# Kernel optimization log

Hardware: AMD Instinct MI355X
Metric: run time of the kernel (lower is better)

The kernel has to match this reference:

```python
import jax, jax.numpy as jnp
import numpy as np

LATENT = 1024
HIDDEN = 4096
ENC = 1024
HEADS = 16
HEAD_DIM = LATENT // HEADS
B, SQ, SK = 4, 1024, 1024
EPS = 1e-5


def _linear(x, w, b):
    # torch nn.Linear: y = x @ w.T + b, w shape (out, in)
    return jnp.einsum('bsi,oi->bso', x, w) + b


def _mha(Q, K, wq, bq, wk, bk, wv, bv, wo, bo):
    Bq, Sq, _ = Q.shape
    Sk = K.shape[1]
    Qp = _linear(Q, wq, bq).reshape(Bq, Sq, HEADS, HEAD_DIM)
    Kp = _linear(K, wk, bk).reshape(Bq, Sk, HEADS, HEAD_DIM)
    Vp = _linear(K, wv, bv).reshape(Bq, Sk, HEADS, HEAD_DIM)
    # NOTE: original scales by 1/sqrt(latent_size), not 1/sqrt(head_dim)
    E = jnp.einsum('bqhd,bkhd->bhqk', Qp, Kp) / np.sqrt(LATENT).astype(np.float32)
    A = jax.nn.softmax(E, axis=-1)
    O = jnp.einsum('bhqk,bkhd->bqhd', A, Vp).reshape(Bq, Sq, LATENT)
    return _linear(O, wo, bo)


def _ln(x, g, b):
    mu = jnp.mean(x, axis=-1, keepdims=True)
    var = jnp.mean((x - mu) ** 2, axis=-1, keepdims=True)
    return (x - mu) * jax.lax.rsqrt(var + EPS) * g + b


def setup_inputs() -> dict:
    key = jax.random.key(0)
    ks = jax.random.split(key, 32)
    s = 0.02
    d = {
        'Q': jax.random.normal(ks[0], (B, SQ, LATENT), jnp.float32),
        'K': jax.random.normal(ks[1], (B, SK, ENC), jnp.float32),
        'a1_wq': jax.random.normal(ks[2], (LATENT, LATENT)) * s,
        'a1_bq': jnp.zeros((LATENT,)),
        'a1_wk': jax.random.normal(ks[3], (LATENT, LATENT)) * s,
        'a1_bk': jnp.zeros((LATENT,)),
        'a1_wv': jax.random.normal(ks[4], (LATENT, LATENT)) * s,
        'a1_bv': jnp.zeros((LATENT,)),
        'a1_wo': jax.random.normal(ks[5], (LATENT, LATENT)) * s,
        'a1_bo': jnp.zeros((LATENT,)),
        'a2_wq': jax.random.normal(ks[6], (LATENT, LATENT)) * s,
        'a2_bq': jnp.zeros((LATENT,)),
        'a2_wk': jax.random.normal(ks[7], (LATENT, ENC)) * s,
        'a2_bk': jnp.zeros((LATENT,)),
        'a2_wv': jax.random.normal(ks[8], (LATENT, ENC)) * s,
        'a2_bv': jnp.zeros((LATENT,)),
        'a2_wo': jax.random.normal(ks[9], (LATENT, LATENT)) * s,
        'a2_bo': jnp.zeros((LATENT,)),
        'fc_w1': jax.random.normal(ks[10], (HIDDEN, LATENT)) * s,
        'fc_b1': jnp.zeros((HIDDEN,)),
        'fc_w2': jax.random.normal(ks[11], (LATENT, HIDDEN)) * s,
        'fc_b2': jnp.zeros((LATENT,)),
        'ln0_g': jnp.ones((LATENT,)), 'ln0_b': jnp.zeros((LATENT,)),
        'ln1_g': jnp.ones((LATENT,)), 'ln1_b': jnp.zeros((LATENT,)),
        'ln2_g': jnp.ones((LATENT,)), 'ln2_b': jnp.zeros((LATENT,)),
    }
    return d


def reference(Q, K, a1_wq, a1_bq, a1_wk, a1_bk, a1_wv, a1_bv, a1_wo, a1_bo,
              a2_wq, a2_bq, a2_wk, a2_bk, a2_wv, a2_bv, a2_wo, a2_bo,
              fc_w1, fc_b1, fc_w2, fc_b2,
              ln0_g, ln0_b, ln1_g, ln1_b, ln2_g, ln2_b):
    # self-attention block
    A1 = _mha(Q, Q, a1_wq, a1_bq, a1_wk, a1_bk, a1_wv, a1_bv, a1_wo, a1_bo)
    X = _ln(Q + A1, ln0_g, ln0_b)
    # cross-attention block
    A2 = _mha(X, K, a2_wq, a2_bq, a2_wk, a2_bk, a2_wv, a2_bv, a2_wo, a2_bo)
    X = _ln(X + A2, ln1_g, ln1_b)
    # FFN: Linear -> ReLU -> Linear
    FC = _linear(jax.nn.relu(_linear(X, fc_w1, fc_b1)), fc_w2, fc_b2)
    X = _ln(X + FC, ln2_g, ln2_b)
    return X
```

## Files before the change

### kernel.cpp

```cpp
#include <hip/hip_runtime.h>
#include <hip/hip_bf16.h>
#include <math.h>

#define LATENT 1024
#define HIDDEN 4096
#define HEADS 16
#define HEAD_DIM 64
#define BATCH 4
#define SQL 1024
#define SKL 1024

typedef __bf16 bf16;
typedef __attribute__((ext_vector_type(4))) __bf16 bf16x4;
typedef __attribute__((ext_vector_type(8))) __bf16 bf16x8;
typedef __attribute__((ext_vector_type(4))) float f32x4;

#define MFMA16 __builtin_amdgcn_mfma_f32_16x16x32_bf16

__device__ __forceinline__ void async_ld16(const bf16* g, bf16* l) {
    __builtin_amdgcn_global_load_lds(
        (const __attribute__((address_space(1))) unsigned int*)g,
        (__attribute__((address_space(3))) unsigned int*)l,
        16, 0, 0);
}

__global__ void detect_dtype(const void* g, int* flag) {
    if (threadIdx.x == 0) *flag = (*(const float*)g == 1.0f) ? 1 : 0;
}

struct CanonArgs {
    const void* src[28];
    bf16* dst[28];
    int n[28];
};

__global__ __launch_bounds__(256) void canonicalize(CanonArgs a, const int* flagp) {
    const int buf = blockIdx.y;
    const int n = a.n[buf];
    const int i0 = (blockIdx.x * 256 + threadIdx.x) * 8;
    if (i0 >= n) return;
    bf16* dst = a.dst[buf];
    if (*flagp) {
        const float* s = (const float*)a.src[buf];
        float4 u0 = *(const float4*)(s + i0);
        float4 u1 = *(const float4*)(s + i0 + 4);
        bf16x8 o;
        o[0] = (bf16)u0.x; o[1] = (bf16)u0.y; o[2] = (bf16)u0.z; o[3] = (bf16)u0.w;
        o[4] = (bf16)u1.x; o[5] = (bf16)u1.y; o[6] = (bf16)u1.z; o[7] = (bf16)u1.w;
        *(bf16x8*)(dst + i0) = o;
    } else {
        *(bf16x8*)(dst + i0) = *(const bf16x8*)((const bf16*)a.src[buf] + i0);
    }
}

template<int BN, bool RELU>
__global__ __launch_bounds__(256, 2)
void gemm2(const bf16* __restrict__ A, const bf16* __restrict__ W,
           const bf16* __restrict__ bias,
           bf16* __restrict__ out0, bf16* __restrict__ out1, bf16* __restrict__ outT,
           int M, int N, int K, int nNormal, int ostride) {
    constexpr int WAVES_N = BN / 64;
    constexpr int WAVES_M = 4 / WAVES_N;
    constexpr int WM = 128 / WAVES_M;
    constexpr int MI = WM / 16;
    constexpr int BROWS = BN / 4;
    constexpr int BUFSZ = (128 + BN) * 64;
    __shared__ alignas(16) bf16 smem[2 * BUFSZ];
    const int tid  = threadIdx.x;
    const int w    = tid >> 6;
    const int lane = tid & 63;
    const int quad = lane >> 4;
    const int l16  = lane & 15;
    const int bm = blockIdx.y * 128;
    const int bn = blockIdx.x * BN;
    const int wr = w / WAVES_N, wc = w % WAVES_N;

    f32x4 acc[MI][4] = {};

    const int srow = lane >> 3;
    const int schk = (lane & 7) * 8;
    const bf16* Abase = A + (long)(bm + w * 32 + srow) * K + schk;
    const bf16* Wbase = W + (long)(bn + w * BROWS + srow) * K + schk;
    const int lAoff = (w * 32 + srow) * 64 + schk;
    const int lBoff = 128 * 64 + (w * BROWS + srow) * 64 + schk;

#define STAGE_G(bufp, kk)                                                      \
    {                                                                          \
        bf16* bb_ = smem + (bufp) * BUFSZ;                                     \
        _Pragma("unroll")                                                      \
        for (int i_ = 0; i_ < 4; ++i_)                                         \
            async_ld16(Abase + (kk) + (long)(i_ * 8) * K, bb_ + lAoff + i_ * 8 * 64); \
        _Pragma("unroll")                                                      \
        for (int i_ = 0; i_ < BROWS / 8; ++i_)                                 \
            async_ld16(Wbase + (kk) + (long)(i_ * 8) * K, bb_ + lBoff + i_ * 8 * 64); \
    }

    STAGE_G(0, 0);
    __asm__ volatile("s_waitcnt vmcnt(0)" ::: "memory");
    __builtin_amdgcn_s_barrier();
    __builtin_amdgcn_sched_barrier(0);

    int cur = 0;
    for (int k0 = 0; k0 < K; k0 += 64) {
        if (k0 + 64 < K) STAGE_G(cur ^ 1, k0 + 64);
        const bf16* lA = smem + cur * BUFSZ;
        const bf16* lB = lA + 128 * 64;
#pragma unroll
        for (int ks = 0; ks < 2; ++ks) {
            bf16x8 af[MI], bfv[4];
#pragma unroll
            for (int i = 0; i < MI; ++i)
                af[i] = *(const bf16x8*)&lA[(wr * WM + i * 16 + l16) * 64 + ks * 32 + quad * 8];
#pragma unroll
            for (int j = 0; j < 4; ++j)
                bfv[j] = *(const bf16x8*)&lB[(wc * 64 + j * 16 + l16) * 64 + ks * 32 + quad * 8];
#pragma unroll
            for (int i = 0; i < MI; ++i)
#pragma unroll
                for (int j = 0; j < 4; ++j)
                    acc[i][j] = MFMA16(af[i], bfv[j], acc[i][j], 0, 0, 0);
        }
        __asm__ volatile("s_waitcnt vmcnt(0)" ::: "memory");
        __builtin_amdgcn_s_barrier();
        __builtin_amdgcn_sched_barrier(0);
        cur ^= 1;
    }
#undef STAGE_G

    float bvv[4];
#pragma unroll
    for (int j = 0; j < 4; ++j) bvv[j] = (float)bias[bn + wc * 64 + j * 16 + l16];

    if (bn < nNormal) {
        bf16* base = out0;
        int colb = bn;
        if (out1 && colb >= 1024) { base = out1; colb -= 1024; }
#pragma unroll
        for (int i = 0; i < MI; ++i) {
#pragma unroll
            for (int r = 0; r < 4; ++r) {
                const int row = bm + wr * WM + i * 16 + quad * 4 + r;
#pragma unroll
                for (int j = 0; j < 4; ++j) {
                    float v = acc[i][j][r] + bvv[j];
                    if (RELU) v = fmaxf(v, 0.f);
                    base[(long)row * ostride + colb + wc * 64 + j * 16 + l16] = (bf16)v;
                }
            }
        }
    } else {
        const int n0v = bn - nNormal;
        __syncthreads();
#pragma unroll
        for (int p = 0; p < 2; ++p) {
            if (p) __syncthreads();
            if (wc == p) {
#pragma unroll
                for (int i = 0; i < MI; ++i)
#pragma unroll
                    for (int j = 0; j < 4; ++j) {
                        const int colL = j * 16 + l16;
                        const int rowL = wr * WM + i * 16 + quad * 4;
                        bf16x4 pk;
#pragma unroll
                        for (int r = 0; r < 4; ++r) pk[r] = (bf16)(acc[i][j][r] + bvv[j]);
                        *(bf16x4*)&smem[colL * 136 + rowL] = pk;
                    }
            }
            __syncthreads();
#pragma unroll
            for (int k = 0; k < 8; ++k) {
                const int c = tid + k * 256;
                const int rL = c >> 5, ch = c & 31;
                *(bf16x4*)&outT[(long)(n0v + p * 64 + rL) * M + bm + ch * 4] =
                    *(const bf16x4*)&smem[rL * 136 + ch * 4];
            }
        }
    }
}

__global__ __launch_bounds__(256, 3)
void attn2(const bf16* __restrict__ Qp, const bf16* __restrict__ Kp,
           const bf16* __restrict__ Vt, bf16* __restrict__ O) {
    __shared__ alignas(16) bf16 lQ[64 * 64];
    __shared__ alignas(16) bf16 lK[2][64 * 64];
    __shared__ alignas(16) bf16 lV[2][64 * 64];
    __shared__ alignas(16) bf16 lP[4][16 * 64];
    const int tid  = threadIdx.x;
    const int w    = tid >> 6;
    const int lane = tid & 63;
    const int quad = lane >> 4;
    const int l16  = lane & 15;
    const int b  = blockIdx.z;
    const int h  = blockIdx.y;
    const int q0 = blockIdx.x * 64;

#pragma unroll
    for (int s = 0; s < 2; ++s) {
        const int c = w * 128 + s * 64 + lane;
        const int row = c >> 3, ch = (c & 7) * 8;
        async_ld16(Qp + (long)(b * SQL + q0 + row) * LATENT + h * 64 + ch, lQ + c * 8);
    }
#define STAGE_KV(buf, kt)                                                        \
    {                                                                            \
        _Pragma("unroll")                                                        \
        for (int s = 0; s < 2; ++s) {                                            \
            const int c = w * 128 + s * 64 + lane;                               \
            const int row = c >> 3, ch = (c & 7) * 8;                            \
            async_ld16(Kp + (long)(b * SKL + (kt) * 64 + row) * LATENT + h * 64 + ch, \
                       &lK[buf][c * 8]);                                         \
            async_ld16(Vt + (long)(h * 64 + row) * (BATCH * SKL) + b * SKL + (kt) * 64 + ch, \
                       &lV[buf][c * 8]);                                         \
        }                                                                        \
    }
    STAGE_KV(0, 0);
    __syncthreads();

    bf16x8 aq[2];
    aq[0] = *(const bf16x8*)&lQ[(w * 16 + l16) * 64 + quad * 8];
    aq[1] = *(const bf16x8*)&lQ[(w * 16 + l16) * 64 + 32 + quad * 8];

    f32x4 o_acc[4] = {};
    float lsum[4] = {0.f, 0.f, 0.f, 0.f};

    for (int kt = 0; kt < SKL / 64; ++kt) {
        const int cur = kt & 1;
        if (kt < SKL / 64 - 1) STAGE_KV(cur ^ 1, kt + 1);

        f32x4 s4[4] = {};
#pragma unroll
        for (int ks = 0; ks < 2; ++ks)
#pragma unroll
            for (int j = 0; j < 4; ++j) {
                bf16x8 bk = *(const bf16x8*)&lK[cur][(j * 16 + l16) * 64 + ks * 32 + quad * 8];
                s4[j] = MFMA16(aq[ks], bk, s4[j], 0, 0, 0);
            }

#pragma unroll
        for (int r = 0; r < 4; ++r)
#pragma unroll
            for (int j = 0; j < 4; ++j) {
                const float p = __expf(s4[j][r] * 0.03125f);
                lsum[r] += p;
                lP[w][(quad * 4 + r) * 64 + j * 16 + l16] = (bf16)p;
            }
        __asm__ volatile("s_waitcnt lgkmcnt(0)" ::: "memory");

#pragma unroll
        for (int ks = 0; ks < 2; ++ks) {
            bf16x8 ap = *(const bf16x8*)&lP[w][l16 * 64 + ks * 32 + quad * 8];
#pragma unroll
            for (int j = 0; j < 4; ++j) {
                bf16x8 bv = *(const bf16x8*)&lV[cur][(j * 16 + l16) * 64 + ks * 32 + quad * 8];
                o_acc[j] = MFMA16(ap, bv, o_acc[j], 0, 0, 0);
            }
        }
        __syncthreads();
    }

#pragma unroll
    for (int r = 0; r < 4; ++r) {
#pragma unroll
        for (int off = 1; off <= 8; off <<= 1)
            lsum[r] += __shfl_xor(lsum[r], off, 64);
    }
#pragma unroll
    for (int r = 0; r < 4; ++r) {
        const float inv = 1.f / lsum[r];
        const int row = q0 + w * 16 + quad * 4 + r;
#pragma unroll
        for (int j = 0; j < 4; ++j)
            O[(long)(b * SQL + row) * LATENT + h * 64 + j * 16 + l16] = (bf16)(o_acc[j][r] * inv);
    }
#undef STAGE_KV
}

template<bool F32OUT>
__global__ __launch_bounds__(256)
void ln_kernel(const bf16* __restrict__ res, const bf16* __restrict__ y,
               const bf16* __restrict__ g, const bf16* __restrict__ bta,
               bf16* __restrict__ outres, void* __restrict__ outb) {
    const int row = blockIdx.x;
    const int tid = threadIdx.x;
    const long base = (long)row * LATENT;
    const int c = tid * 4;
    bf16x4 rv = *(const bf16x4*)&res[base + c];
    bf16x4 yv = *(const bf16x4*)&y[base + c];
    float x[4];
    float s1 = 0.f, s2 = 0.f;
#pragma unroll
    for (int i = 0; i < 4; ++i) {
        float v = (float)rv[i] + (float)yv[i];
        x[i] = v; s1 += v; s2 += v * v;
    }
#pragma unroll
    for (int off = 32; off >= 1; off >>= 1) {
        s1 += __shfl_xor(s1, off, 64);
        s2 += __shfl_xor(s2, off, 64);
    }
    __shared__ float ps1[4], ps2[4];
    const int w = tid >> 6, lane = tid & 63;
    if (lane == 0) { ps1[w] = s1; ps2[w] = s2; }
    __syncthreads();
    s1 = ps1[0] + ps1[1] + ps1[2] + ps1[3];
    s2 = ps2[0] + ps2[1] + ps2[2] + ps2[3];
    const float mu = s1 * (1.f / LATENT);
    const float var = s2 * (1.f / LATENT) - mu * mu;
    const float rstd = rsqrtf(var + 1e-5f);
    bf16x4 gv = *(const bf16x4*)&g[c];
    bf16x4 bv = *(const bf16x4*)&bta[c];
    float o[4];
#pragma unroll
    for (int i = 0; i < 4; ++i)
        o[i] = (x[i] - mu) * rstd * (float)gv[i] + (float)bv[i];
    if (F32OUT) {
        float4 f; f.x = o[0]; f.y = o[1]; f.z = o[2]; f.w = o[3];
        *(float4*)&((float*)outb)[base + c] = f;
    } else {
        bf16x4 bo;
#pragma unroll
        for (int i = 0; i < 4; ++i) bo[i] = (bf16)o[i];
        *(bf16x4*)&((bf16*)outb)[base + c] = bo;
        if (outres) *(bf16x4*)&outres[base + c] = bo;
    }
}

extern "C" void kernel_launch(void* const* d_in, const int* in_sizes, int n_in,
                              void* d_out, int out_size, void* d_ws, size_t ws_size,
                              hipStream_t stream) {
    char* ws = (char*)d_ws;

    static const int order[28] = {2, 4, 6, 3, 5, 7, 12, 14, 13, 15,
                                  0, 1, 8, 9, 10, 11, 16, 17, 18, 19,
                                  20, 21, 22, 23, 24, 25, 26, 27};
    size_t coff[28];
    size_t cur = 256;
    for (int k = 0; k < 28; ++k) {
        const int i = order[k];
        coff[i] = cur;
        cur += (((size_t)in_sizes[i] * 2) + 255) & ~(size_t)255;
    }
    const size_t canon_end = (cur + 255) & ~(size_t)255;
    const size_t MB8 = 8ull << 20;
    const size_t need = canon_end + 7 * MB8;
    const bool full = ws_size >= need;

    const bf16* cv[28];
    if (full) {
        int* flag = (int*)ws;
        detect_dtype<<<dim3(1), dim3(64), 0, stream>>>(d_in[22], flag);
        CanonArgs ca;
        for (int i = 0; i < 28; ++i) {
            ca.src[i] = d_in[i];
            ca.dst[i] = (bf16*)(ws + coff[i]);
            ca.n[i]   = in_sizes[i];
            cv[i]     = (const bf16*)(ws + coff[i]);
        }
        canonicalize<<<dim3(2048, 28), dim3(256), 0, stream>>>(ca, flag);
    } else {
        for (int i = 0; i < 28; ++i) cv[i] = (const bf16*)d_in[i];
    }

    const size_t base = full ? canon_end : 0;
    bf16* Xres = (bf16*)(ws + base);
    bf16* Yf   = (bf16*)(ws + base + 1 * MB8);
    bf16* Xb   = (bf16*)(ws + base + 2 * MB8);
    bf16* Qp   = (bf16*)(ws + base + 3 * MB8);
    bf16* Kp   = (bf16*)(ws + base + 4 * MB8);
    bf16* Vt   = (bf16*)(ws + base + 5 * MB8);
    bf16* AttO = (bf16*)(ws + base + 6 * MB8);
    bf16* H    = Qp;

    const bf16 *Qc = cv[0], *Kc = cv[1];
    const int M = BATCH * SQL;
    dim3 blk(256);
    dim3 ga(SQL / 64, HEADS, BATCH);

    gemm2<128, false><<<dim3(3072 / 128, M / 128), blk, 0, stream>>>(
        Qc, cv[2], cv[3], Qp, Kp, Vt, M, 3072, LATENT, 2048, 1024);
    attn2<<<ga, blk, 0, stream>>>(Qp, Kp, Vt, AttO);
    gemm2<64, false><<<dim3(1024 / 64, M / 128), blk, 0, stream>>>(
        AttO, cv[8], cv[9], Yf, nullptr, nullptr, M, 1024, LATENT, 1024, 1024);
    ln_kernel<false><<<dim3(M), blk, 0, stream>>>(Qc, Yf, cv[22], cv[23], Xres, Xb);

    gemm2<64, false><<<dim3(1024 / 64, M / 128), blk, 0, stream>>>(
        Xb, cv[10], cv[11], Qp, nullptr, nullptr, M, 1024, LATENT, 1024, 1024);
    gemm2<128, false><<<dim3(2048 / 128, M / 128), blk, 0, stream>>>(
        Kc, cv[12], cv[13], Kp, nullptr, Vt, M, 2048, LATENT, 1024, 1024);
    attn2<<<ga, blk, 0, stream>>>(Qp, Kp, Vt, AttO);
    gemm2<64, false><<<dim3(1024 / 64, M / 128), blk, 0, stream>>>(
        AttO, cv[16], cv[17], Yf, nullptr, nullptr, M, 1024, LATENT, 1024, 1024);
    ln_kernel<false><<<dim3(M), blk, 0, stream>>>(Xres, Yf, cv[24], cv[25], Xres, Xb);

    gemm2<128, true><<<dim3(4096 / 128, M / 128), blk, 0, stream>>>(
        Xb, cv[18], cv[19], H, nullptr, nullptr, M, HIDDEN, LATENT, 4096, 4096);
    gemm2<64, false><<<dim3(1024 / 64, M / 128), blk, 0, stream>>>(
        H, cv[20], cv[21], Yf, nullptr, nullptr, M, 1024, HIDDEN, 1024, 1024);
    ln_kernel<true><<<dim3(M), blk, 0, stream>>>(Xres, Yf, cv[26], cv[27], nullptr, d_out);
}
```

Measured before the change: 520.5 us.

## Triple-buffer GEMM K-loop with 32-wide swizzled LDS tiles and higher occupancy

Restructures the bf16 GEMM main loop to use BK=32 tiles in a three-stage ring of LDS buffers. Each thread issues async global-to-LDS loads two stages ahead and waits with partial vmcnt counts, so loads overlap compute instead of draining every iteration. LDS rows are XOR-swizzled to avoid bank conflicts on the MFMA fragment reads. Launch bounds are raised to 3-4 blocks per CU. The trade-off is twice as many barriers per K, plus register pressure under the tighter occupancy bound.

```diff
diff --git a/kernel.cpp b/kernel.cpp
--- a/kernel.cpp
+++ b/kernel.cpp
@@ -54,8 +54,8 @@
 }
 
 template<int BN, bool RELU>
-__global__ __launch_bounds__(256, 2)
-void gemm2(const bf16* __restrict__ A, const bf16* __restrict__ W,
+__global__ __launch_bounds__(256, (BN == 128) ? 3 : 4)
+void gemm4(const bf16* __restrict__ A, const bf16* __restrict__ W,
            const bf16* __restrict__ bias,
            bf16* __restrict__ out0, bf16* __restrict__ out1, bf16* __restrict__ outT,
            int M, int N, int K, int nNormal, int ostride) {
@@ -63,9 +63,12 @@
     constexpr int WAVES_M = 4 / WAVES_N;
     constexpr int WM = 128 / WAVES_M;
     constexpr int MI = WM / 16;
-    constexpr int BROWS = BN / 4;
-    constexpr int BUFSZ = (128 + BN) * 64;
-    __shared__ alignas(16) bf16 smem[2 * BUFSZ];
+    constexpr int ASLOT = 128 * 4;
+    constexpr int BSLOT = BN * 4;
+    constexpr int SLOTS = ASLOT + BSLOT;
+    constexpr int LPT   = SLOTS / 256;
+    constexpr int BUFE  = SLOTS * 8;
+    __shared__ alignas(16) bf16 smem[3 * BUFE];
     const int tid  = threadIdx.x;
     const int w    = tid >> 6;
     const int lane = tid & 63;
@@ -77,53 +80,71 @@
 
     f32x4 acc[MI][4] = {};
 
-    const int srow = lane >> 3;
-    const int schk = (lane & 7) * 8;
-    const bf16* Abase = A + (long)(bm + w * 32 + srow) * K + schk;
-    const bf16* Wbase = W + (long)(bn + w * BROWS + srow) * K + schk;
-    const int lAoff = (w * 32 + srow) * 64 + schk;
-    const int lBoff = 128 * 64 + (w * BROWS + srow) * 64 + schk;
-
-#define STAGE_G(bufp, kk)                                                      \
+    const bf16* gsrc[LPT]; int loff[LPT];
+#pragma unroll
+    for (int i = 0; i < LPT; ++i) {
+        const int s = tid + i * 256;
+        int row, cs;
+        const bf16* base;
+        if (s < ASLOT) { row = s >> 2;           cs = s & 3; base = A + (long)(bm + row) * K; }
+        else           { const int sb = s - ASLOT; row = sb >> 2; cs = sb & 3;
+                         base = W + (long)(bn + row) * K; }
+        const int cg = cs ^ ((row >> 1) & 3);
+        gsrc[i] = base + cg * 8;
+        loff[i] = s * 8;
+    }
+
+    int offA[MI], offB[4];
+#pragma unroll
+    for (int i = 0; i < MI; ++i) {
+        const int r = wr * WM + i * 16 + l16;
+        offA[i] = r * 32 + ((quad ^ ((r >> 1) & 3)) << 3);
+    }
+#pragma unroll
+    for (int j = 0; j < 4; ++j) {
+        const int r = wc * 64 + j * 16 + l16;
+        offB[j] = ASLOT * 8 + r * 32 + ((quad ^ ((r >> 1) & 3)) << 3);
+    }
+
+#define STAGE_G(dst, tt)                                                       \
     {                                                                          \
-        bf16* bb_ = smem + (bufp) * BUFSZ;                                     \
         _Pragma("unroll")                                                      \
-        for (int i_ = 0; i_ < 4; ++i_)                                         \
-            async_ld16(Abase + (kk) + (long)(i_ * 8) * K, bb_ + lAoff + i_ * 8 * 64); \
-        _Pragma("unroll")                                                      \
-        for (int i_ = 0; i_ < BROWS / 8; ++i_)                                 \
-            async_ld16(Wbase + (kk) + (long)(i_ * 8) * K, bb_ + lBoff + i_ * 8 * 64); \
-    }
-
-    STAGE_G(0, 0);
-    __asm__ volatile("s_waitcnt vmcnt(0)" ::: "memory");
+        for (int i_ = 0; i_ < LPT; ++i_)                                       \
+            async_ld16(gsrc[i_] + (tt) * 32, (dst) + loff[i_]);                \
+    }
+
+    const int NK = K >> 5;
+    bf16 *p0 = smem, *p1 = smem + BUFE, *p2 = smem + 2 * BUFE;
+    STAGE_G(p0, 0);
+    STAGE_G(p1, 1);
+    if constexpr (BN == 128) __asm__ volatile("s_waitcnt vmcnt(4)" ::: "memory");
+    else                     __asm__ volatile("s_waitcnt vmcnt(3)" ::: "memory");
     __builtin_amdgcn_s_barrier();
     __builtin_amdgcn_sched_barrier(0);
 
-    int cur = 0;
-    for (int k0 = 0; k0 < K; k0 += 64) {
-        if (k0 + 64 < K) STAGE_G(cur ^ 1, k0 + 64);
-        const bf16* lA = smem + cur * BUFSZ;
-        const bf16* lB = lA + 128 * 64;
-#pragma unroll
-        for (int ks = 0; ks < 2; ++ks) {
-            bf16x8 af[MI], bfv[4];
-#pragma unroll
-            for (int i = 0; i < MI; ++i)
-                af[i] = *(const bf16x8*)&lA[(wr * WM + i * 16 + l16) * 64 + ks * 32 + quad * 8];
+    for (int t = 0; t < NK; ++t) {
+        if (t + 2 < NK) STAGE_G(p2, t + 2);
+        bf16x8 af[MI], bfv[4];
+#pragma unroll
+        for (int i = 0; i < MI; ++i) af[i]  = *(const bf16x8*)&p0[offA[i]];
+#pragma unroll
+        for (int j = 0; j < 4; ++j) bfv[j] = *(const bf16x8*)&p0[offB[j]];
+#pragma unroll
+        for (int i = 0; i < MI; ++i)
 #pragma unroll
             for (int j = 0; j < 4; ++j)
-                bfv[j] = *(const bf16x8*)&lB[(wc * 64 + j * 16 + l16) * 64 + ks * 32 + quad * 8];
-#pragma unroll
-            for (int i = 0; i < MI; ++i)
-#pragma unroll
-                for (int j = 0; j < 4; ++j)
-                    acc[i][j] = MFMA16(af[i], bfv[j], acc[i][j], 0, 0, 0);
-        }
-        __asm__ volatile("s_waitcnt vmcnt(0)" ::: "memory");
-        __builtin_amdgcn_s_barrier();
-        __builtin_amdgcn_sched_barrier(0);
-        cur ^= 1;
+                acc[i][j] = MFMA16(af[i], bfv[j], acc[i][j], 0, 0, 0);
+        if (t + 2 < NK) {
+            if constexpr (BN == 128) __asm__ volatile("s_waitcnt vmcnt(4)" ::: "memory");
+            else                     __asm__ volatile("s_waitcnt vmcnt(3)" ::: "memory");
+        } else if (t + 1 < NK) {
+            __asm__ volatile("s_waitcnt vmcnt(0)" ::: "memory");
+        }
+        if (t + 1 < NK) {
+            __builtin_amdgcn_s_barrier();
+            __builtin_amdgcn_sched_barrier(0);
+        }
+        bf16* tp = p0; p0 = p1; p1 = p2; p2 = tp;
     }
 #undef STAGE_G
 
@@ -376,25 +397,25 @@
     dim3 blk(256);
     dim3 ga(SQL / 64, HEADS, BATCH);
 
-    gemm2<128, false><<<dim3(3072 / 128, M / 128), blk, 0, stream>>>(
+    gemm4<128, false><<<dim3(3072 / 128, M / 128), blk, 0, stream>>>(
         Qc, cv[2], cv[3], Qp, Kp, Vt, M, 3072, LATENT, 2048, 1024);
     attn2<<<ga, blk, 0, stream>>>(Qp, Kp, Vt, AttO);
-    gemm2<64, false><<<dim3(1024 / 64, M / 128), blk, 0, stream>>>(
+    gemm4<64, false><<<dim3(1024 / 64, M / 128), blk, 0, stream>>>(
         AttO, cv[8], cv[9], Yf, nullptr, nullptr, M, 1024, LATENT, 1024, 1024);
     ln_kernel<false><<<dim3(M), blk, 0, stream>>>(Qc, Yf, cv[22], cv[23], Xres, Xb);
 
-    gemm2<64, false><<<dim3(1024 / 64, M / 128), blk, 0, stream>>>(
+    gemm4<64, false><<<dim3(1024 / 64, M / 128), blk, 0, stream>>>(
         Xb, cv[10], cv[11], Qp, nullptr, nullptr, M, 1024, LATENT, 1024, 1024);
-    gemm2<128, false><<<dim3(2048 / 128, M / 128), blk, 0, stream>>>(
+    gemm4<128, false><<<dim3(2048 / 128, M / 128), blk, 0, stream>>>(
         Kc, cv[12], cv[13], Kp, nullptr, Vt, M, 2048, LATENT, 1024, 1024);
     attn2<<<ga, blk, 0, stream>>>(Qp, Kp, Vt, AttO);
-    gemm2<64, false><<<dim3(1024 / 64, M / 128), blk, 0, stream>>>(
+    gemm4<64, false><<<dim3(1024 / 64, M / 128), blk, 0, stream>>>(
         AttO, cv[16], cv[17], Yf, nullptr, nullptr, M, 1024, LATENT, 1024, 1024);
     ln_kernel<false><<<dim3(M), blk, 0, stream>>>(Xres, Yf, cv[24], cv[25], Xres, Xb);
 
-    gemm2<128, true><<<dim3(4096 / 128, M / 128), blk, 0, stream>>>(
+    gemm4<128, true><<<dim3(4096 / 128, M / 128), blk, 0, stream>>>(
         Xb, cv[18], cv[19], H, nullptr, nullptr, M, HIDDEN, LATENT, 4096, 4096);
-    gemm2<64, false><<<dim3(1024 / 64, M / 128), blk, 0, stream>>>(
+    gemm4<64, false><<<dim3(1024 / 64, M / 128), blk, 0, stream>>>(
         H, cv[20], cv[21], Yf, nullptr, nullptr, M, 1024, HIDDEN, 1024, 1024);
     ln_kernel<true><<<dim3(M), blk, 0, stream>>>(Xres, Yf, cv[26], cv[27], nullptr, d_out);
 }
```

Measured after the change: 520.4 us. About the same (-0.0%).

## Add 128x256 triple-buffered GEMM kernel for wide projection and FFN-up GEMMs

Applied to the files above, without the earlier changes.

Adds a new GEMM kernel with 128x256 output tiles, K-step 32, three LDS stages filled by async global-to-LDS loads, XOR-swizzled LDS layout, and an XCD-aware block remap. It replaces the 128x128 gemm2 for the fused QKV projection, the cross-attention KV projection and the FFN first layer. The larger tile raises arithmetic intensity per loaded byte, and deeper buffering aims to hide memory latency. In exchange it uses more accumulator registers (128 floats per thread) and gives fewer workgroups for the 2048-wide GEMM.

```diff
diff --git a/kernel.cpp b/kernel.cpp
--- a/kernel.cpp
+++ b/kernel.cpp
@@ -50,6 +50,153 @@
         *(bf16x8*)(dst + i0) = o;
     } else {
         *(bf16x8*)(dst + i0) = *(const bf16x8*)((const bf16*)a.src[buf] + i0);
+    }
+}
+
+template<bool RELU>
+__global__ __launch_bounds__(256, 2)
+void gemm8(const bf16* __restrict__ A, const bf16* __restrict__ W,
+           const bf16* __restrict__ bias,
+           bf16* __restrict__ out0, bf16* __restrict__ out1, bf16* __restrict__ outT,
+           int M, int N, int K, int nNormal, int ostride) {
+    constexpr int AE   = 128 * 32;
+    constexpr int BE   = 256 * 32;
+    constexpr int BUFE = AE + BE;
+    __shared__ alignas(16) bf16 smem[3 * BUFE];
+    const int tid  = threadIdx.x;
+    const int w    = tid >> 6;
+    const int lane = tid & 63;
+    const int quad = lane >> 4;
+    const int l16  = lane & 15;
+    const int wrr  = w >> 1, wcc = w & 1;
+    const int nx  = gridDim.x;
+    const int nwg = nx * gridDim.y;
+    int bid = blockIdx.y * nx + blockIdx.x;
+    bid = (bid & 7) * (nwg >> 3) + (bid >> 3);
+    const int bm = (bid / nx) * 128;
+    const int bn = (bid % nx) * 256;
+
+    f32x4 acc[4][8] = {};
+
+    const bf16* gsrc[6]; int loff[6];
+#pragma unroll
+    for (int i = 0; i < 6; ++i) {
+        const int s = tid + i * 256;
+        if (s < 512) {
+            const int r = s >> 2, cs = s & 3;
+            gsrc[i] = A + (long)(bm + r) * K + ((cs ^ ((r >> 1) & 3)) << 3);
+            loff[i] = s * 8;
+        } else {
+            const int sb = s - 512;
+            const int r = sb >> 2, cs = sb & 3;
+            gsrc[i] = W + (long)(bn + r) * K + ((cs ^ ((r >> 1) & 3)) << 3);
+            loff[i] = AE + sb * 8;
+        }
+    }
+
+    int offA[4], offB[8];
+#pragma unroll
+    for (int i = 0; i < 4; ++i) {
+        const int r = wrr * 64 + i * 16 + l16;
+        offA[i] = r * 32 + ((quad ^ ((r >> 1) & 3)) << 3);
+    }
+#pragma unroll
+    for (int j = 0; j < 8; ++j) {
+        const int r = wcc * 128 + j * 16 + l16;
+        offB[j] = AE + r * 32 + ((quad ^ ((r >> 1) & 3)) << 3);
+    }
+
+#define STAGE_W(dst, tt)                                                       \
+    {                                                                          \
+        _Pragma("unroll")                                                      \
+        for (int i_ = 0; i_ < 6; ++i_)                                         \
+            async_ld16(gsrc[i_] + (tt) * 32, (dst) + loff[i_]);                \
+    }
+
+    const int NK = K >> 5;
+    bf16 *p0 = smem, *p1 = smem + BUFE, *p2 = smem + 2 * BUFE;
+    STAGE_W(p0, 0);
+    STAGE_W(p1, 1);
+    __asm__ volatile("s_waitcnt vmcnt(6)" ::: "memory");
+    __builtin_amdgcn_s_barrier();
+    __builtin_amdgcn_sched_barrier(0);
+
+    for (int t = 0; t < NK; ++t) {
+        if (t + 2 < NK) STAGE_W(p2, t + 2);
+        bf16x8 af[4], bfv[8];
+#pragma unroll
+        for (int i = 0; i < 4; ++i) af[i]  = *(const bf16x8*)&p0[offA[i]];
+#pragma unroll
+        for (int j = 0; j < 8; ++j) bfv[j] = *(const bf16x8*)&p0[offB[j]];
+#pragma unroll
+        for (int j = 0; j < 8; ++j)
+#pragma unroll
+            for (int i = 0; i < 4; ++i)
+                acc[i][j] = MFMA16(af[i], bfv[j], acc[i][j], 0, 0, 0);
+        if (t + 2 < NK) {
+            __asm__ volatile("s_waitcnt vmcnt(6)" ::: "memory");
+        } else if (t + 1 < NK) {
+            __asm__ volatile("s_waitcnt vmcnt(0)" ::: "memory");
+        }
+        if (t + 1 < NK) {
+            __builtin_amdgcn_s_barrier();
+            __builtin_amdgcn_sched_barrier(0);
+        }
+        bf16* tp = p0; p0 = p1; p1 = p2; p2 = tp;
+    }
+#undef STAGE_W
+
+    float bvv[8];
+#pragma unroll
+    for (int j = 0; j < 8; ++j) bvv[j] = (float)bias[bn + wcc * 128 + j * 16 + l16];
+
+    if (bn < nNormal) {
+#pragma unroll
+        for (int j = 0; j < 8; ++j) {
+            const int colj = bn + wcc * 128 + j * 16;
+            bf16* basej = out0;
+            int cb = colj;
+            if (out1 && cb >= 1024) { basej = out1; cb -= 1024; }
+#pragma unroll
+            for (int i = 0; i < 4; ++i) {
+#pragma unroll
+                for (int r = 0; r < 4; ++r) {
+                    const int row = bm + wrr * 64 + i * 16 + quad * 4 + r;
+                    float v = acc[i][j][r] + bvv[j];
+                    if (RELU) v = fmaxf(v, 0.f);
+                    basej[(long)row * ostride + cb + l16] = (bf16)v;
+                }
+            }
+        }
+    } else {
+        const int n0v = bn - nNormal;
+        __syncthreads();
+#pragma unroll
+        for (int p = 0; p < 4; ++p) {
+            if (p) __syncthreads();
+            if (wcc == (p >> 1)) {
+#pragma unroll
+                for (int i = 0; i < 4; ++i)
+#pragma unroll
+                    for (int jl = 0; jl < 4; ++jl) {
+                        const int j = (p & 1) * 4 + jl;
+                        const int colL = jl * 16 + l16;
+                        const int rowL = wrr * 64 + i * 16 + quad * 4;
+                        bf16x4 pk;
+#pragma unroll
+                        for (int r = 0; r < 4; ++r) pk[r] = (bf16)(acc[i][j][r] + bvv[j]);
+                        *(bf16x4*)&smem[colL * 136 + rowL] = pk;
+                    }
+            }
+            __syncthreads();
+#pragma unroll
+            for (int k = 0; k < 8; ++k) {
+                const int c = tid + k * 256;
+                const int rT = c >> 5, ch = c & 31;
+                *(bf16x4*)&outT[(long)(n0v + p * 64 + rT) * M + bm + ch * 4] =
+                    *(const bf16x4*)&smem[rT * 136 + ch * 4];
+            }
+        }
     }
 }
 
@@ -376,7 +523,7 @@
     dim3 blk(256);
     dim3 ga(SQL / 64, HEADS, BATCH);
 
-    gemm2<128, false><<<dim3(3072 / 128, M / 128), blk, 0, stream>>>(
+    gemm8<false><<<dim3(3072 / 256, M / 128), blk, 0, stream>>>(
         Qc, cv[2], cv[3], Qp, Kp, Vt, M, 3072, LATENT, 2048, 1024);
     attn2<<<ga, blk, 0, stream>>>(Qp, Kp, Vt, AttO);
     gemm2<64, false><<<dim3(1024 / 64, M / 128), blk, 0, stream>>>(
@@ -385,14 +532,14 @@
 
     gemm2<64, false><<<dim3(1024 / 64, M / 128), blk, 0, stream>>>(
         Xb, cv[10], cv[11], Qp, nullptr, nullptr, M, 1024, LATENT, 1024, 1024);
-    gemm2<128, false><<<dim3(2048 / 128, M / 128), blk, 0, stream>>>(
+    gemm8<false><<<dim3(2048 / 256, M / 128), blk, 0, stream>>>(
         Kc, cv[12], cv[13], Kp, nullptr, Vt, M, 2048, LATENT, 1024, 1024);
     attn2<<<ga, blk, 0, stream>>>(Qp, Kp, Vt, AttO);
     gemm2<64, false><<<dim3(1024 / 64, M / 128), blk, 0, stream>>>(
         AttO, cv[16], cv[17], Yf, nullptr, nullptr, M, 1024, LATENT, 1024, 1024);
     ln_kernel<false><<<dim3(M), blk, 0, stream>>>(Xres, Yf, cv[24], cv[25], Xres, Xb);
 
-    gemm2<128, true><<<dim3(4096 / 128, M / 128), blk, 0, stream>>>(
+    gemm8<true><<<dim3(4096 / 256, M / 128), blk, 0, stream>>>(
         Xb, cv[18], cv[19], H, nullptr, nullptr, M, HIDDEN, LATENT, 4096, 4096);
     gemm2<64, false><<<dim3(1024 / 64, M / 128), blk, 0, stream>>>(
         H, cv[20], cv[21], Yf, nullptr, nullptr, M, 1024, HIDDEN, 1024, 1024);
```

After: 515.8 us. Within noise of the previous version (-0.9%).
